# Kernel optimization log

Measured on AMD Instinct MI355X. Metric: run time of the kernel, lower is better.

Reference implementation:

```python
import jax, jax.numpy as jnp
import numpy as np

# config dims (see shape_source)
NO = 8        # Max_Object
NT = 32       # Max_Time
C = 512       # feat_dims
VD = 1024     # visual_dim
RD = 300      # self.nfeat (relation word-vector dim)
H = 4         # headnum
B = 8         # batch
No = NT * 2 * NO      # 512 object-graph nodes
Nr = NT * NO * NO     # 2048 relation-graph nodes


def _glorot(key, shape):
    fan_in = shape[0]
    return jax.random.normal(key, shape, dtype=jnp.float32) / np.sqrt(fan_in)


def setup_inputs() -> dict:
    key = jax.random.key(0)
    ks = jax.random.split(key, 18)
    inp = {
        "Ao": jax.random.uniform(ks[0], (B, No, No), dtype=jnp.float32),
        "srco": jax.random.normal(ks[1], (B, 1, 1, No, VD), dtype=jnp.float32),
        "Ar": jax.random.uniform(ks[2], (B, Nr, Nr), dtype=jnp.float32),
        "srcr": jax.random.normal(ks[3], (B, 1, 1, Nr, RD), dtype=jnp.float32),
        # GraphConvolution weights: gcl_o/gcl2_o and gcl_r/gcl2_r
        "Wo1": _glorot(ks[4], (VD, 1024)),
        "Wo2": _glorot(ks[5], (1024, C)),
        "Wr1": _glorot(ks[6], (RD, 1024)),
        "Wr2": _glorot(ks[7], (1024, C)),
        # MultiHeadAttention (e2n) projections
        "Wq": _glorot(ks[8], (C, C)), "bq": jnp.zeros((C,), jnp.float32),
        "Wk": _glorot(ks[9], (C, C)), "bk": jnp.zeros((C,), jnp.float32),
        "Wv": _glorot(ks[10], (C, C)), "bv": jnp.zeros((C,), jnp.float32),
        "Wp": _glorot(ks[11], (C, C)), "bp": jnp.zeros((C,), jnp.float32),
        # e2n_embed: Linear(2C -> C)
        "We": _glorot(ks[12], (2 * C, C)), "be": jnp.zeros((C,), jnp.float32),
    }
    return inp


def _gcn2(A, x, W1, W2):
    """Two stacked GraphConvolution layers with self-loops: relu((A+I) @ x @ W).
    A: (b,N,N), x: (b,N,Din). Vectorized over batch (torch code loops per-sample)."""
    eye = jnp.eye(A.shape[-1], dtype=A.dtype)
    Ah = A + eye
    h = jax.nn.relu(jnp.einsum('bij,bjd->bid', Ah, x @ W1))
    return jax.nn.relu(jnp.einsum('bij,bjd->bid', Ah, h @ W2))


def _mha(x, Wq, bq, Wk, bk, Wv, bv, Wp, bp):
    """Standard multi-head self-attention. x: (Bseg, S, C)."""
    Bs, S, _ = x.shape
    dh = C // H
    q = (x @ Wq + bq).reshape(Bs, S, H, dh)
    k = (x @ Wk + bk).reshape(Bs, S, H, dh)
    v = (x @ Wv + bv).reshape(Bs, S, H, dh)
    attn = jax.nn.softmax(jnp.einsum('bqhd,bkhd->bhqk', q, k) / np.sqrt(dh), axis=-1)
    o = jnp.einsum('bhqk,bkhd->bqhd', attn, v).reshape(Bs, S, C)
    return o @ Wp + bp


def _forward(Ao, srco, Ar, srcr, Wo1, Wo2, Wr1, Wr2,
             Wq, bq, Wk, bk, Wv, bv, Wp, bp, We, be):
    b = Ao.shape[0]
    # object-graph GCN (torch loops over batch; vectorized here)
    xo = srco[:, 0, 0, :, :VD]                       # (b, No, VD)
    srco_gcn = _gcn2(Ao, xo, Wo1, Wo2)               # (b, No, C)
    out_gcn_o = srco_gcn.reshape(b, NT, 2 * NO, C)
    # relation-graph GCN
    xr = srcr[:, 0, 0]                               # (b, Nr, RD)
    srcr_gcn = _gcn2(Ar, xr, Wr1, Wr2)               # (b, Nr, C)
    out_gcn_r = srcr_gcn.reshape(b, NT, NO * NO, C)
    # compute_e2n: segment-wise MHA over NO-token windows (torch loops over NO)
    r = out_gcn_r.reshape(b * NT, NO, NO, C)
    seg_a = r.reshape(b * NT * NO, NO, C)                      # rows of NOxNO grid
    a = _mha(seg_a, Wq, bq, Wk, bk, Wv, bv, Wp, bp).mean(axis=1)
    a = a.reshape(b * NT, NO, C)
    seg_o = jnp.swapaxes(r, 1, 2).reshape(b * NT * NO, NO, C)  # cols (permute 0,2,1,3)
    o = _mha(seg_o, Wq, bq, Wk, bk, Wv, bv, Wp, bp).mean(axis=1)
    o = o.reshape(b * NT, NO, C)
    tmp = jnp.concatenate([a, o], axis=1)                      # (b*NT, 2*NO, C)
    cat = jnp.concatenate([tmp, out_gcn_o.reshape(b * NT, 2 * NO, C)], axis=-1)
    out_e2n = cat @ We + be
    return out_e2n.reshape(b, NT, 2 * NO, C)


def reference(Ao, srco, Ar, srcr, Wo1, Wo2, Wr1, Wr2,
              Wq, bq, Wk, bk, Wv, bv, Wp, bp, We, be):
    return _forward(Ao, srco, Ar, srcr, Wo1, Wo2, Wr1, Wr2,
                    Wq, bq, Wk, bk, Wv, bv, Wp, bp, We, be)
```

## Files before the change

### kernel.cpp

```cpp
#include <hip/hip_runtime.h>
#include <hip/hip_bf16.h>


typedef __attribute__((ext_vector_type(4))) float f32x4;
typedef __attribute__((ext_vector_type(8))) short bf16x8s;

#define TILE 128
#define BKK 32
#define LDSS 40

__device__ inline void split2(float a, float b, unsigned& h, unsigned& l) {
    __hip_bfloat16 ha = __float2bfloat16(a), hb = __float2bfloat16(b);
    float ra = __bfloat162float(ha), rb = __bfloat162float(hb);
    __hip_bfloat16 la = __float2bfloat16(a - ra), lb = __float2bfloat16(b - rb);
    unsigned short uha = *(unsigned short*)&ha, uhb = *(unsigned short*)&hb;
    unsigned short ula = *(unsigned short*)&la, ulb = *(unsigned short*)&lb;
    h = (unsigned)uha | ((unsigned)uhb << 16);
    l = (unsigned)ula | ((unsigned)ulb << 16);
}

__global__ __launch_bounds__(256) void gemm_split2(
    const float* __restrict__ A, long long sA, int lda,
    const float* __restrict__ BT, long long sBT, int ldbt,
    float* __restrict__ D, long long sD, int ldd,
    const float* __restrict__ addN, long long sAddN, int ldaddN,
    const float* __restrict__ addT, long long sAddT, int ldaddT,
    const float* __restrict__ bias,
    int K, int relu)
{
    __shared__ __hip_bfloat16 Ah[TILE * LDSS], Al[TILE * LDSS];
    __shared__ __hip_bfloat16 Bh[TILE * LDSS], Bl[TILE * LDSS];

    const int tid  = threadIdx.x;
    const int lane = tid & 63;
    const int wave = tid >> 6;
    const int wm   = (wave >> 1) * 64;
    const int wn   = (wave & 1) * 64;
    const int row0 = blockIdx.y * TILE;
    const int col0 = blockIdx.x * TILE;
    const int b    = blockIdx.z;

    const float* Ab = A  + (size_t)b * sA;
    const float* Bb = BT + (size_t)b * sBT;

    f32x4 acc[4][4];
#pragma unroll
    for (int i = 0; i < 4; ++i)
#pragma unroll
        for (int j = 0; j < 4; ++j) acc[i][j] = (f32x4){0.f, 0.f, 0.f, 0.f};

    const int quad = lane >> 4;
    const int l16  = lane & 15;

    for (int k0 = 0; k0 < K; k0 += BKK) {
        __syncthreads();
#pragma unroll
        for (int it = 0; it < 2; ++it) {
            int task = tid + it * 256;
            int m = task >> 2, kq = task & 3;
            const float* ap = Ab + (size_t)(row0 + m) * lda + k0 + kq * 8;
            float4 v0 = *(const float4*)ap;
            float4 v1 = *(const float4*)(ap + 4);
            uint4 H, L;
            split2(v0.x, v0.y, H.x, L.x); split2(v0.z, v0.w, H.y, L.y);
            split2(v1.x, v1.y, H.z, L.z); split2(v1.z, v1.w, H.w, L.w);
            *(uint4*)(&Ah[m * LDSS + kq * 8]) = H;
            *(uint4*)(&Al[m * LDSS + kq * 8]) = L;
        }
#pragma unroll
        for (int it = 0; it < 2; ++it) {
            int task = tid + it * 256;
            int n = task >> 2, kq = task & 3;
            const float* bp = Bb + (size_t)(col0 + n) * ldbt + k0 + kq * 8;
            float4 v0 = *(const float4*)bp;
            float4 v1 = *(const float4*)(bp + 4);
            uint4 H, L;
            split2(v0.x, v0.y, H.x, L.x); split2(v0.z, v0.w, H.y, L.y);
            split2(v1.x, v1.y, H.z, L.z); split2(v1.z, v1.w, H.w, L.w);
            *(uint4*)(&Bh[n * LDSS + kq * 8]) = H;
            *(uint4*)(&Bl[n * LDSS + kq * 8]) = L;
        }
        __syncthreads();

        bf16x8s ah[4], al[4], bh[4], bl[4];
#pragma unroll
        for (int mt = 0; mt < 4; ++mt) {
            int r = (wm + mt * 16 + l16) * LDSS + quad * 8;
            ah[mt] = *(const bf16x8s*)(&Ah[r]);
            al[mt] = *(const bf16x8s*)(&Al[r]);
        }
#pragma unroll
        for (int nt = 0; nt < 4; ++nt) {
            int r = (wn + nt * 16 + l16) * LDSS + quad * 8;
            bh[nt] = *(const bf16x8s*)(&Bh[r]);
            bl[nt] = *(const bf16x8s*)(&Bl[r]);
        }
#pragma unroll
        for (int mt = 0; mt < 4; ++mt)
#pragma unroll
            for (int nt = 0; nt < 4; ++nt) {
                acc[mt][nt] = __builtin_amdgcn_mfma_f32_16x16x32_bf16(ah[mt], bh[nt], acc[mt][nt], 0, 0, 0);
                acc[mt][nt] = __builtin_amdgcn_mfma_f32_16x16x32_bf16(ah[mt], bl[nt], acc[mt][nt], 0, 0, 0);
                acc[mt][nt] = __builtin_amdgcn_mfma_f32_16x16x32_bf16(al[mt], bh[nt], acc[mt][nt], 0, 0, 0);
            }
    }

    float* Db = D + (size_t)b * sD;
    const float* AddN = addN ? addN + (size_t)b * sAddN : nullptr;
    const float* AddT = addT ? addT + (size_t)b * sAddT : nullptr;
#pragma unroll
    for (int mt = 0; mt < 4; ++mt)
#pragma unroll
        for (int nt = 0; nt < 4; ++nt)
#pragma unroll
            for (int r = 0; r < 4; ++r) {
                int m = row0 + wm + mt * 16 + quad * 4 + r;
                int n = col0 + wn + nt * 16 + l16;
                float v = acc[mt][nt][r];
                if (AddN) v += AddN[(size_t)m * ldaddN + n];
                if (AddT) v += AddT[(size_t)n * ldaddT + m];
                if (bias) v += bias[n];
                if (relu && v < 0.f) v = 0.f;
                Db[(size_t)m * ldd + n] = v;
            }
}

__global__ __launch_bounds__(256) void padtrans(
    const float* __restrict__ src, float* __restrict__ dst,
    int R, int C, int Rp, int Cp)
{
    __shared__ float T[64][65];
    const int t = threadIdx.x;
    const int tr = t >> 4, tc = t & 15;
    const int c0 = blockIdx.x * 64, r0 = blockIdx.y * 64;
    const size_t bat = blockIdx.z;
    const float* sb = src + bat * (size_t)R * C;
    float* db = dst + bat * (size_t)Cp * Rp;

#pragma unroll
    for (int i = 0; i < 4; ++i) {
        int rr = tr + i * 16;
        int gr = r0 + rr;
        float v0 = 0.f, v1 = 0.f, v2 = 0.f, v3 = 0.f;
        if (gr < R) {
            int c = c0 + tc * 4;
            const float* s = sb + (size_t)gr * C + c;
            if (c + 0 < C) v0 = s[0];
            if (c + 1 < C) v1 = s[1];
            if (c + 2 < C) v2 = s[2];
            if (c + 3 < C) v3 = s[3];
        }
        T[rr][tc * 4 + 0] = v0; T[rr][tc * 4 + 1] = v1;
        T[rr][tc * 4 + 2] = v2; T[rr][tc * 4 + 3] = v3;
    }
    __syncthreads();
#pragma unroll
    for (int i = 0; i < 4; ++i) {
        int cc = tr + i * 16;
        float4 v = { T[tc * 4 + 0][cc], T[tc * 4 + 1][cc],
                     T[tc * 4 + 2][cc], T[tc * 4 + 3][cc] };
        *(float4*)(db + (size_t)(c0 + cc) * Rp + r0 + tc * 4) = v;
    }
}

__global__ __launch_bounds__(256) void gemm_bf16(
    const __hip_bfloat16* __restrict__ A, long long sA, int lda,
    const __hip_bfloat16* __restrict__ B, long long sB, int ldb,
    void* __restrict__ D, long long sD, int ldd,
    const __hip_bfloat16* __restrict__ addsrc, long long sAdd, int ldadd,
    const float* __restrict__ bias,
    int K, int relu, int outF32)
{
    __shared__ __hip_bfloat16 As[TILE * LDSS];
    __shared__ __hip_bfloat16 Bs[TILE * LDSS];

    const int tid  = threadIdx.x;
    const int lane = tid & 63;
    const int wave = tid >> 6;
    const int wm   = (wave >> 1) * 64;
    const int wn   = (wave & 1) * 64;
    const int row0 = blockIdx.y * TILE;
    const int col0 = blockIdx.x * TILE;
    const int b    = blockIdx.z;

    const __hip_bfloat16* Ab = A + (size_t)b * sA;
    const __hip_bfloat16* Bb = B + (size_t)b * sB;

    f32x4 acc[4][4];
#pragma unroll
    for (int i = 0; i < 4; ++i)
#pragma unroll
        for (int j = 0; j < 4; ++j) acc[i][j] = (f32x4){0.f, 0.f, 0.f, 0.f};

    const int quad = lane >> 4;
    const int l16  = lane & 15;

    for (int k0 = 0; k0 < K; k0 += BKK) {
        __syncthreads();
#pragma unroll
        for (int it = 0; it < 2; ++it) {
            int task = tid + it * 256;
            int m = task >> 2, kq = task & 3;
            uint4 val = *(const uint4*)(Ab + (size_t)(row0 + m) * lda + k0 + kq * 8);
            *(uint4*)(&As[m * LDSS + kq * 8]) = val;
        }
#pragma unroll
        for (int it = 0; it < 2; ++it) {
            int task = tid + it * 256;
            int kk = task >> 4, n8 = task & 15;
            uint4 val = *(const uint4*)(Bb + (size_t)(k0 + kk) * ldb + col0 + n8 * 8);
            const __hip_bfloat16* v16 = (const __hip_bfloat16*)&val;
#pragma unroll
            for (int u = 0; u < 8; ++u)
                Bs[(n8 * 8 + u) * LDSS + kk] = v16[u];
        }
        __syncthreads();

        bf16x8s afrag[4], bfrag[4];
#pragma unroll
        for (int mt = 0; mt < 4; ++mt)
            afrag[mt] = *(const bf16x8s*)(&As[(wm + mt * 16 + l16) * LDSS + quad * 8]);
#pragma unroll
        for (int nt = 0; nt < 4; ++nt)
            bfrag[nt] = *(const bf16x8s*)(&Bs[(wn + nt * 16 + l16) * LDSS + quad * 8]);
#pragma unroll
        for (int mt = 0; mt < 4; ++mt)
#pragma unroll
            for (int nt = 0; nt < 4; ++nt)
                acc[mt][nt] = __builtin_amdgcn_mfma_f32_16x16x32_bf16(
                    afrag[mt], bfrag[nt], acc[mt][nt], 0, 0, 0);
    }

    __hip_bfloat16* Db16 = (__hip_bfloat16*)D + (size_t)b * sD;
    float*          DbF  = (float*)D + (size_t)b * sD;
    const __hip_bfloat16* Addb = addsrc ? addsrc + (size_t)b * sAdd : nullptr;
#pragma unroll
    for (int mt = 0; mt < 4; ++mt)
#pragma unroll
        for (int nt = 0; nt < 4; ++nt)
#pragma unroll
            for (int r = 0; r < 4; ++r) {
                int m = row0 + wm + mt * 16 + quad * 4 + r;
                int n = col0 + wn + nt * 16 + l16;
                float v = acc[mt][nt][r];
                if (Addb) v += __bfloat162float(Addb[(size_t)m * ldadd + n]);
                if (bias) v += bias[n];
                if (relu && v < 0.f) v = 0.f;
                if (outF32) DbF[(size_t)m * ldd + n] = v;
                else        Db16[(size_t)m * ldd + n] = __float2bfloat16(v);
            }
}

__global__ void convert_kernel(const float* __restrict__ src,
                               __hip_bfloat16* __restrict__ dst, int n4)
{
    int i = blockIdx.x * blockDim.x + threadIdx.x;
    if (i >= n4) return;
    float4 v = ((const float4*)src)[i];
    __hip_bfloat16 t0 = __float2bfloat16(v.x), t1 = __float2bfloat16(v.y);
    __hip_bfloat16 t2 = __float2bfloat16(v.z), t3 = __float2bfloat16(v.w);
    ushort4 o = { *(unsigned short*)&t0, *(unsigned short*)&t1,
                  *(unsigned short*)&t2, *(unsigned short*)&t3 };
    ((ushort4*)dst)[i] = o;
}

__global__ __launch_bounds__(256) void attn_kernel(
    const float* __restrict__ q,
    const float* __restrict__ k,
    const float* __restrict__ v,
    __hip_bfloat16* __restrict__ abar)
{
    __shared__ float qs[8][512], ks[8][512], vs[8][512];
    __shared__ float sc[4][8][8];
    __shared__ float wb[4][8];

    const int tid  = threadIdx.x;
    const int mode = blockIdx.y;
    const int g    = blockIdx.x >> 3;
    const int idx  = blockIdx.x & 7;
    const int rowBase = g * 64;

    for (int t = tid; t < 512; t += 256) {
        int p = t >> 6, c8 = (t & 63) * 8;
        int row = (mode == 0) ? (rowBase + idx * 8 + p) : (rowBase + p * 8 + idx);
        const float* qp = q + (size_t)row * 512 + c8;
        const float* kp = k + (size_t)row * 512 + c8;
        const float* vp = v + (size_t)row * 512 + c8;
        *(float4*)(&qs[p][c8])     = *(const float4*)(qp);
        *(float4*)(&qs[p][c8 + 4]) = *(const float4*)(qp + 4);
        *(float4*)(&ks[p][c8])     = *(const float4*)(kp);
        *(float4*)(&ks[p][c8 + 4]) = *(const float4*)(kp + 4);
        *(float4*)(&vs[p][c8])     = *(const float4*)(vp);
        *(float4*)(&vs[p][c8 + 4]) = *(const float4*)(vp + 4);
    }
    __syncthreads();

    {
        int h = tid >> 6, l = tid & 63;
        int i = l >> 3, j = l & 7;
        const float* qrow = &qs[i][h * 128];
        const float* krow = &ks[j][h * 128];
        float s = 0.f;
#pragma unroll
        for (int d = 0; d < 128; d += 4) {
            float4 qa = *(const float4*)(qrow + d);
            float4 kb = *(const float4*)(krow + d);
            s += qa.x * kb.x + qa.y * kb.y + qa.z * kb.z + qa.w * kb.w;
        }
        sc[h][i][j] = s * 0.08838834764831845f;
    }
    __syncthreads();

    if (tid < 32) {
        int h = tid >> 3, i = tid & 7;
        float mx = -1e30f;
#pragma unroll
        for (int j = 0; j < 8; ++j) mx = fmaxf(mx, sc[h][i][j]);
        float e[8], sum = 0.f;
#pragma unroll
        for (int j = 0; j < 8; ++j) { e[j] = __expf(sc[h][i][j] - mx); sum += e[j]; }
        float inv = 1.f / sum;
#pragma unroll
        for (int j = 0; j < 8; ++j) sc[h][i][j] = e[j] * inv;
    }
    __syncthreads();

    if (tid < 32) {
        int h = tid >> 3, j = tid & 7;
        float s = 0.f;
#pragma unroll
        for (int i = 0; i < 8; ++i) s += sc[h][i][j];
        wb[h][j] = s * 0.125f;
    }
    __syncthreads();

    {
        int orow = g * 16 + mode * 8 + idx;
        for (int c = tid; c < 512; c += 256) {
            int h = c >> 7;
            float o = 0.f;
#pragma unroll
            for (int j = 0; j < 8; ++j) o += wb[h][j] * vs[j][c];
            abar[(size_t)orow * 512 + c] = __float2bfloat16(o);
        }
    }
}


extern "C" void kernel_launch(void* const* d_in, const int* in_sizes, int n_in,
                              void* d_out, int out_size, void* d_ws, size_t ws_size,
                              hipStream_t stream)
{
    const float* Ao   = (const float*)d_in[0];
    const float* srco = (const float*)d_in[1];
    const float* Ar   = (const float*)d_in[2];
    const float* srcr = (const float*)d_in[3];
    const float* Wo1  = (const float*)d_in[4];
    const float* Wo2  = (const float*)d_in[5];
    const float* Wr1  = (const float*)d_in[6];
    const float* Wr2  = (const float*)d_in[7];
    const float* Wq   = (const float*)d_in[8];
    const float* bq   = (const float*)d_in[9];
    const float* Wk   = (const float*)d_in[10];
    const float* bk   = (const float*)d_in[11];
    const float* Wv   = (const float*)d_in[12];
    const float* bv   = (const float*)d_in[13];
    const float* Wp   = (const float*)d_in[14];
    const float* bp   = (const float*)d_in[15];
    const float* We   = (const float*)d_in[16];
    const float* be   = (const float*)d_in[17];
    float* out = (float*)d_out;

    char* ws = (char*)d_ws;
    const size_t R0 = 0;
    const size_t R1 = 67108864;
    const size_t R2 = 100663296;
    const size_t R3 = 134217728;
    const size_t R4 = 167772160;
    const size_t R5 = 192937984;

    float* HRf  = (float*)(ws + R0);
    float* qF   = (float*)(ws + R0);
    float* kF   = (float*)(ws + R0 + 33554432);
    float* T2Rf = (float*)(ws + R1);
    float* vF   = (float*)(ws + R1);
    float* Uf   = (float*)(ws + R2);
    float* T2RT = (float*)(ws + R2);
    float* GRf  = (float*)(ws + R3);
    float* XPT  = (float*)(ws + R4);
    __hip_bfloat16* ABAR = (__hip_bfloat16*)(ws + R4);
    float* WPT  = (float*)(ws + R5);
    float* Wr2T = (float*)(ws + R5 + 1310720);
    float* WqT  = (float*)(ws + R5 + 3407872);
    float* WkT  = (float*)(ws + R5 + 4456448);
    float* WvT  = (float*)(ws + R5 + 5505024);

    __hip_bfloat16* TO    = (__hip_bfloat16*)(ws + R2 + 0);
    __hip_bfloat16* HO    = (__hip_bfloat16*)(ws + R2 + 8388608);
    __hip_bfloat16* T2O   = (__hip_bfloat16*)(ws + R2 + 16777216);
    __hip_bfloat16* CAT   = (__hip_bfloat16*)(ws + R2 + 20971520);
    __hip_bfloat16* srcoB = (__hip_bfloat16*)(ws + R2 + 29360128);
    __hip_bfloat16* AoB   = (__hip_bfloat16*)(ws + R2 + 37748736);
    __hip_bfloat16* Wo1B  = (__hip_bfloat16*)(ws + R2 + 41943040);
    __hip_bfloat16* Wo2B  = (__hip_bfloat16*)(ws + R2 + 44040192);
    __hip_bfloat16* WeB   = (__hip_bfloat16*)(ws + R2 + 45088768);
    __hip_bfloat16* WpB   = (__hip_bfloat16*)(ws + R2 + 46137344);

    dim3 blk(256);
    auto cvt = [&](const float* s, __hip_bfloat16* d, int n) {
        convert_kernel<<<dim3((n / 4 + 255) / 256), blk, 0, stream>>>(s, d, n / 4);
    };

    padtrans<<<dim3(6, 32, 8), blk, 0, stream>>>(srcr, XPT, 2048, 300, 2048, 384);
    padtrans<<<dim3(16, 5, 1), blk, 0, stream>>>(Wr1, WPT, 300, 1024, 320, 1024);
    padtrans<<<dim3(8, 16, 1), blk, 0, stream>>>(Wr2, Wr2T, 1024, 512, 1024, 512);
    padtrans<<<dim3(8, 8, 1), blk, 0, stream>>>(Wq, WqT, 512, 512, 512, 512);
    padtrans<<<dim3(8, 8, 1), blk, 0, stream>>>(Wk, WkT, 512, 512, 512, 512);
    padtrans<<<dim3(8, 8, 1), blk, 0, stream>>>(Wv, WvT, 512, 512, 512, 512);

    gemm_split2<<<dim3(3, 16, 8), blk, 0, stream>>>(
        Ar, 2048LL * 2048, 2048, XPT, 384LL * 2048, 2048,
        Uf, 2048LL * 384, 384, nullptr, 0, 0, XPT, 384LL * 2048, 2048,
        nullptr, 2048, 0);
    gemm_split2<<<dim3(8, 128, 1), blk, 0, stream>>>(
        Uf, 0, 384, WPT, 0, 320,
        HRf, 0, 1024, nullptr, 0, 0, nullptr, 0, 0,
        nullptr, 320, 1);
    gemm_split2<<<dim3(4, 128, 1), blk, 0, stream>>>(
        HRf, 0, 1024, Wr2T, 0, 1024,
        T2Rf, 0, 512, nullptr, 0, 0, nullptr, 0, 0,
        nullptr, 1024, 0);
    padtrans<<<dim3(8, 32, 8), blk, 0, stream>>>(T2Rf, T2RT, 2048, 512, 2048, 512);
    gemm_split2<<<dim3(4, 16, 8), blk, 0, stream>>>(
        Ar, 2048LL * 2048, 2048, T2RT, 512LL * 2048, 2048,
        GRf, 2048LL * 512, 512, T2Rf, 2048LL * 512, 512, nullptr, 0, 0,
        nullptr, 2048, 1);
    gemm_split2<<<dim3(4, 128, 1), blk, 0, stream>>>(
        GRf, 0, 512, WqT, 0, 512, qF, 0, 512,
        nullptr, 0, 0, nullptr, 0, 0, bq, 512, 0);
    gemm_split2<<<dim3(4, 128, 1), blk, 0, stream>>>(
        GRf, 0, 512, WkT, 0, 512, kF, 0, 512,
        nullptr, 0, 0, nullptr, 0, 0, bk, 512, 0);
    gemm_split2<<<dim3(4, 128, 1), blk, 0, stream>>>(
        GRf, 0, 512, WvT, 0, 512, vF, 0, 512,
        nullptr, 0, 0, nullptr, 0, 0, bv, 512, 0);
    attn_kernel<<<dim3(2048, 2), blk, 0, stream>>>(qF, kF, vF, ABAR);

    cvt(srco, srcoB, 4194304);
    cvt(Ao, AoB, 2097152);
    cvt(Wo1, Wo1B, 1048576);
    cvt(Wo2, Wo2B, 524288);
    cvt(We, WeB, 524288);
    cvt(Wp, WpB, 262144);
    gemm_bf16<<<dim3(8, 32, 1), blk, 0, stream>>>(srcoB, 0, 1024, Wo1B, 0, 1024,
        TO, 0, 1024, nullptr, 0, 0, nullptr, 1024, 0, 0);
    gemm_bf16<<<dim3(8, 4, 8), blk, 0, stream>>>(AoB, 512LL * 512, 512, TO, 512LL * 1024, 1024,
        HO, 512LL * 1024, 1024, TO, 512LL * 1024, 1024, nullptr, 512, 1, 0);
    gemm_bf16<<<dim3(4, 32, 1), blk, 0, stream>>>(HO, 0, 1024, Wo2B, 0, 512,
        T2O, 0, 512, nullptr, 0, 0, nullptr, 1024, 0, 0);
    gemm_bf16<<<dim3(4, 4, 8), blk, 0, stream>>>(AoB, 512LL * 512, 512, T2O, 512LL * 512, 512,
        (void*)(CAT + 512), 512LL * 1024, 1024, T2O, 512LL * 512, 512, nullptr, 512, 1, 0);
    gemm_bf16<<<dim3(4, 32, 1), blk, 0, stream>>>(ABAR, 0, 512, WpB, 0, 512,
        CAT, 0, 1024, nullptr, 0, 0, bp, 512, 0, 0);
    gemm_bf16<<<dim3(4, 32, 1), blk, 0, stream>>>(CAT, 0, 1024, WeB, 0, 512,
        out, 0, 512, nullptr, 0, 0, be, 1024, 0, 1);
}
```

Measured before the change: 1.203 ms.

## Pre-split fp32 operands into bf16 hi/lo planes and drop V precision

Replaces the fp32-loading split GEMM with a kernel that reads precomputed bf16 high/low planes, so the costly float-to-bf16 splitting happens once per element instead of once per tile reload. Intermediate GEMM outputs are written directly as hi/lo planes, and the T2R transpose now moves 16-bit data. The V projection switches to a plain single-bf16 GEMM on the high plane only, which reduces work but lowers precision for V. Splitting Ar up front adds an extra pass over the large 2048x2048 batched matrix and enlarges the workspace.

Measured after the change: 1.258 ms. +4.6%, slower.

```diff
diff --git a/kernel.cpp b/kernel.cpp
--- a/kernel.cpp
+++ b/kernel.cpp
@@ -9,27 +9,31 @@
 #define BKK 32
 #define LDSS 40
 
-__device__ inline void split2(float a, float b, unsigned& h, unsigned& l) {
-    __hip_bfloat16 ha = __float2bfloat16(a), hb = __float2bfloat16(b);
-    float ra = __bfloat162float(ha), rb = __bfloat162float(hb);
-    __hip_bfloat16 la = __float2bfloat16(a - ra), lb = __float2bfloat16(b - rb);
-    unsigned short uha = *(unsigned short*)&ha, uhb = *(unsigned short*)&hb;
-    unsigned short ula = *(unsigned short*)&la, ulb = *(unsigned short*)&lb;
-    h = (unsigned)uha | ((unsigned)uhb << 16);
-    l = (unsigned)ula | ((unsigned)ulb << 16);
-}
-
-__global__ __launch_bounds__(256) void gemm_split2(
-    const float* __restrict__ A, long long sA, int lda,
-    const float* __restrict__ BT, long long sBT, int ldbt,
-    float* __restrict__ D, long long sD, int ldd,
-    const float* __restrict__ addN, long long sAddN, int ldaddN,
-    const float* __restrict__ addT, long long sAddT, int ldaddT,
+__device__ inline void splt(float v, unsigned short& h, unsigned short& l) {
+    __hip_bfloat16 hb = __float2bfloat16(v);
+    float hf = __bfloat162float(hb);
+    __hip_bfloat16 lb = __float2bfloat16(v - hf);
+    h = *(unsigned short*)&hb;
+    l = *(unsigned short*)&lb;
+}
+
+__global__ __launch_bounds__(256) void gemm3p(
+    const __hip_bfloat16* __restrict__ AH, const __hip_bfloat16* __restrict__ AL,
+    long long sA, int lda,
+    const __hip_bfloat16* __restrict__ BTH, const __hip_bfloat16* __restrict__ BTL,
+    long long sBT, int ldbt,
+    float* __restrict__ DF,
+    __hip_bfloat16* __restrict__ DH, __hip_bfloat16* __restrict__ DL,
+    long long sD, int ldd,
+    const __hip_bfloat16* __restrict__ addNH, const __hip_bfloat16* __restrict__ addNL,
+    long long sAddN, int ldaddN,
+    const __hip_bfloat16* __restrict__ addTH, const __hip_bfloat16* __restrict__ addTL,
+    long long sAddT, int ldaddT,
     const float* __restrict__ bias,
     int K, int relu)
 {
-    __shared__ __hip_bfloat16 Ah[TILE * LDSS], Al[TILE * LDSS];
-    __shared__ __hip_bfloat16 Bh[TILE * LDSS], Bl[TILE * LDSS];
+    __shared__ __hip_bfloat16 Ahs[TILE * LDSS], Als[TILE * LDSS];
+    __shared__ __hip_bfloat16 Bhs[TILE * LDSS], Bls[TILE * LDSS];
 
     const int tid  = threadIdx.x;
     const int lane = tid & 63;
@@ -40,8 +44,10 @@
     const int col0 = blockIdx.x * TILE;
     const int b    = blockIdx.z;
 
-    const float* Ab = A  + (size_t)b * sA;
-    const float* Bb = BT + (size_t)b * sBT;
+    const __hip_bfloat16* AHb = AH + (size_t)b * sA;
+    const __hip_bfloat16* ALb = AL + (size_t)b * sA;
+    const __hip_bfloat16* BHb = BTH + (size_t)b * sBT;
+    const __hip_bfloat16* BLb = BTL + (size_t)b * sBT;
 
     f32x4 acc[4][4];
 #pragma unroll
@@ -58,27 +64,17 @@
         for (int it = 0; it < 2; ++it) {
             int task = tid + it * 256;
             int m = task >> 2, kq = task & 3;
-            const float* ap = Ab + (size_t)(row0 + m) * lda + k0 + kq * 8;
-            float4 v0 = *(const float4*)ap;
-            float4 v1 = *(const float4*)(ap + 4);
-            uint4 H, L;
-            split2(v0.x, v0.y, H.x, L.x); split2(v0.z, v0.w, H.y, L.y);
-            split2(v1.x, v1.y, H.z, L.z); split2(v1.z, v1.w, H.w, L.w);
-            *(uint4*)(&Ah[m * LDSS + kq * 8]) = H;
-            *(uint4*)(&Al[m * LDSS + kq * 8]) = L;
+            size_t go = (size_t)(row0 + m) * lda + k0 + kq * 8;
+            *(uint4*)(&Ahs[m * LDSS + kq * 8]) = *(const uint4*)(AHb + go);
+            *(uint4*)(&Als[m * LDSS + kq * 8]) = *(const uint4*)(ALb + go);
         }
 #pragma unroll
         for (int it = 0; it < 2; ++it) {
             int task = tid + it * 256;
             int n = task >> 2, kq = task & 3;
-            const float* bp = Bb + (size_t)(col0 + n) * ldbt + k0 + kq * 8;
-            float4 v0 = *(const float4*)bp;
-            float4 v1 = *(const float4*)(bp + 4);
-            uint4 H, L;
-            split2(v0.x, v0.y, H.x, L.x); split2(v0.z, v0.w, H.y, L.y);
-            split2(v1.x, v1.y, H.z, L.z); split2(v1.z, v1.w, H.w, L.w);
-            *(uint4*)(&Bh[n * LDSS + kq * 8]) = H;
-            *(uint4*)(&Bl[n * LDSS + kq * 8]) = L;
+            size_t go = (size_t)(col0 + n) * ldbt + k0 + kq * 8;
+            *(uint4*)(&Bhs[n * LDSS + kq * 8]) = *(const uint4*)(BHb + go);
+            *(uint4*)(&Bls[n * LDSS + kq * 8]) = *(const uint4*)(BLb + go);
         }
         __syncthreads();
 
@@ -86,14 +82,14 @@
 #pragma unroll
         for (int mt = 0; mt < 4; ++mt) {
             int r = (wm + mt * 16 + l16) * LDSS + quad * 8;
-            ah[mt] = *(const bf16x8s*)(&Ah[r]);
-            al[mt] = *(const bf16x8s*)(&Al[r]);
+            ah[mt] = *(const bf16x8s*)(&Ahs[r]);
+            al[mt] = *(const bf16x8s*)(&Als[r]);
         }
 #pragma unroll
         for (int nt = 0; nt < 4; ++nt) {
             int r = (wn + nt * 16 + l16) * LDSS + quad * 8;
-            bh[nt] = *(const bf16x8s*)(&Bh[r]);
-            bl[nt] = *(const bf16x8s*)(&Bl[r]);
+            bh[nt] = *(const bf16x8s*)(&Bhs[r]);
+            bl[nt] = *(const bf16x8s*)(&Bls[r]);
         }
 #pragma unroll
         for (int mt = 0; mt < 4; ++mt)
@@ -105,9 +101,13 @@
             }
     }
 
-    float* Db = D + (size_t)b * sD;
-    const float* AddN = addN ? addN + (size_t)b * sAddN : nullptr;
-    const float* AddT = addT ? addT + (size_t)b * sAddT : nullptr;
+    float* DFb = DF ? DF + (size_t)b * sD : nullptr;
+    __hip_bfloat16* DHb = DH ? DH + (size_t)b * sD : nullptr;
+    __hip_bfloat16* DLb = DL ? DL + (size_t)b * sD : nullptr;
+    const __hip_bfloat16* aNH = addNH ? addNH + (size_t)b * sAddN : nullptr;
+    const __hip_bfloat16* aNL = addNL ? addNL + (size_t)b * sAddN : nullptr;
+    const __hip_bfloat16* aTH = addTH ? addTH + (size_t)b * sAddT : nullptr;
+    const __hip_bfloat16* aTL = addTL ? addTL + (size_t)b * sAddT : nullptr;
 #pragma unroll
     for (int mt = 0; mt < 4; ++mt)
 #pragma unroll
@@ -117,17 +117,41 @@
                 int m = row0 + wm + mt * 16 + quad * 4 + r;
                 int n = col0 + wn + nt * 16 + l16;
                 float v = acc[mt][nt][r];
-                if (AddN) v += AddN[(size_t)m * ldaddN + n];
-                if (AddT) v += AddT[(size_t)n * ldaddT + m];
+                if (aNH) v += __bfloat162float(aNH[(size_t)m * ldaddN + n])
+                            + __bfloat162float(aNL[(size_t)m * ldaddN + n]);
+                if (aTH) v += __bfloat162float(aTH[(size_t)n * ldaddT + m])
+                            + __bfloat162float(aTL[(size_t)n * ldaddT + m]);
                 if (bias) v += bias[n];
                 if (relu && v < 0.f) v = 0.f;
-                Db[(size_t)m * ldd + n] = v;
+                if (DFb) DFb[(size_t)m * ldd + n] = v;
+                else {
+                    unsigned short h, l;
+                    splt(v, h, l);
+                    ((unsigned short*)DHb)[(size_t)m * ldd + n] = h;
+                    ((unsigned short*)DLb)[(size_t)m * ldd + n] = l;
+                }
             }
 }
 
-__global__ __launch_bounds__(256) void padtrans(
-    const float* __restrict__ src, float* __restrict__ dst,
-    int R, int C, int Rp, int Cp)
+__global__ void split_planes(const float* __restrict__ src,
+                             __hip_bfloat16* __restrict__ H,
+                             __hip_bfloat16* __restrict__ L, int n8)
+{
+    int i = blockIdx.x * blockDim.x + threadIdx.x;
+    if (i >= n8) return;
+    float4 v0 = ((const float4*)src)[i * 2];
+    float4 v1 = ((const float4*)src)[i * 2 + 1];
+    float vals[8] = {v0.x, v0.y, v0.z, v0.w, v1.x, v1.y, v1.z, v1.w};
+    unsigned short hh[8], ll[8];
+#pragma unroll
+    for (int u = 0; u < 8; ++u) splt(vals[u], hh[u], ll[u]);
+    *(uint4*)((unsigned short*)H + (size_t)i * 8) = *(uint4*)hh;
+    *(uint4*)((unsigned short*)L + (size_t)i * 8) = *(uint4*)ll;
+}
+
+__global__ __launch_bounds__(256) void padtrans_split(
+    const float* __restrict__ src, __hip_bfloat16* __restrict__ dH,
+    __hip_bfloat16* __restrict__ dL, int R, int C, int Rp, int Cp)
 {
     __shared__ float T[64][65];
     const int t = threadIdx.x;
@@ -135,7 +159,8 @@
     const int c0 = blockIdx.x * 64, r0 = blockIdx.y * 64;
     const size_t bat = blockIdx.z;
     const float* sb = src + bat * (size_t)R * C;
-    float* db = dst + bat * (size_t)Cp * Rp;
+    unsigned short* dHb = (unsigned short*)dH + bat * (size_t)Cp * Rp;
+    unsigned short* dLb = (unsigned short*)dL + bat * (size_t)Cp * Rp;
 
 #pragma unroll
     for (int i = 0; i < 4; ++i) {
@@ -157,9 +182,42 @@
 #pragma unroll
     for (int i = 0; i < 4; ++i) {
         int cc = tr + i * 16;
-        float4 v = { T[tc * 4 + 0][cc], T[tc * 4 + 1][cc],
-                     T[tc * 4 + 2][cc], T[tc * 4 + 3][cc] };
-        *(float4*)(db + (size_t)(c0 + cc) * Rp + r0 + tc * 4) = v;
+        unsigned short h[4], l[4];
+#pragma unroll
+        for (int u = 0; u < 4; ++u) splt(T[tc * 4 + u][cc], h[u], l[u]);
+        size_t off = (size_t)(c0 + cc) * Rp + r0 + tc * 4;
+        *(ushort4*)(dHb + off) = *(ushort4*)h;
+        *(ushort4*)(dLb + off) = *(ushort4*)l;
+    }
+}
+
+__global__ __launch_bounds__(256) void trans_bf16(
+    const __hip_bfloat16* __restrict__ sH, const __hip_bfloat16* __restrict__ sL,
+    __hip_bfloat16* __restrict__ dH, __hip_bfloat16* __restrict__ dL,
+    int R, int C)
+{
+    __shared__ unsigned short T[64][68];
+    const int plane = blockIdx.z & 1;
+    const size_t bat = blockIdx.z >> 1;
+    const unsigned short* s = (const unsigned short*)(plane ? sL : sH) + bat * (size_t)R * C;
+    unsigned short* d = (unsigned short*)(plane ? dL : dH) + bat * (size_t)R * C;
+    const int t = threadIdx.x;
+    const int tr = t >> 4, tc = t & 15;
+    const int c0 = blockIdx.x * 64, r0 = blockIdx.y * 64;
+#pragma unroll
+    for (int i = 0; i < 4; ++i) {
+        int rr = tr + i * 16;
+        ushort4 v = *(const ushort4*)(s + (size_t)(r0 + rr) * C + c0 + tc * 4);
+        T[rr][tc * 4 + 0] = v.x; T[rr][tc * 4 + 1] = v.y;
+        T[rr][tc * 4 + 2] = v.z; T[rr][tc * 4 + 3] = v.w;
+    }
+    __syncthreads();
+#pragma unroll
+    for (int i = 0; i < 4; ++i) {
+        int cc = tr + i * 16;
+        ushort4 o = { T[tc * 4 + 0][cc], T[tc * 4 + 1][cc],
+                      T[tc * 4 + 2][cc], T[tc * 4 + 3][cc] };
+        *(ushort4*)(d + (size_t)(c0 + cc) * R + r0 + tc * 4) = o;
     }
 }
 
@@ -372,78 +430,91 @@
     float* out = (float*)d_out;
 
     char* ws = (char*)d_ws;
-    const size_t R0 = 0;
-    const size_t R1 = 67108864;
-    const size_t R2 = 100663296;
-    const size_t R3 = 134217728;
-    const size_t R4 = 167772160;
-    const size_t R5 = 192937984;
-
-    float* HRf  = (float*)(ws + R0);
-    float* qF   = (float*)(ws + R0);
-    float* kF   = (float*)(ws + R0 + 33554432);
-    float* T2Rf = (float*)(ws + R1);
-    float* vF   = (float*)(ws + R1);
-    float* Uf   = (float*)(ws + R2);
-    float* T2RT = (float*)(ws + R2);
-    float* GRf  = (float*)(ws + R3);
-    float* XPT  = (float*)(ws + R4);
-    __hip_bfloat16* ABAR = (__hip_bfloat16*)(ws + R4);
-    float* WPT  = (float*)(ws + R5);
-    float* Wr2T = (float*)(ws + R5 + 1310720);
-    float* WqT  = (float*)(ws + R5 + 3407872);
-    float* WkT  = (float*)(ws + R5 + 4456448);
-    float* WvT  = (float*)(ws + R5 + 5505024);
-
-    __hip_bfloat16* TO    = (__hip_bfloat16*)(ws + R2 + 0);
-    __hip_bfloat16* HO    = (__hip_bfloat16*)(ws + R2 + 8388608);
-    __hip_bfloat16* T2O   = (__hip_bfloat16*)(ws + R2 + 16777216);
-    __hip_bfloat16* CAT   = (__hip_bfloat16*)(ws + R2 + 20971520);
-    __hip_bfloat16* srcoB = (__hip_bfloat16*)(ws + R2 + 29360128);
-    __hip_bfloat16* AoB   = (__hip_bfloat16*)(ws + R2 + 37748736);
-    __hip_bfloat16* Wo1B  = (__hip_bfloat16*)(ws + R2 + 41943040);
-    __hip_bfloat16* Wo2B  = (__hip_bfloat16*)(ws + R2 + 44040192);
-    __hip_bfloat16* WeB   = (__hip_bfloat16*)(ws + R2 + 45088768);
-    __hip_bfloat16* WpB   = (__hip_bfloat16*)(ws + R2 + 46137344);
+    __hip_bfloat16* ArH   = (__hip_bfloat16*)(ws + 0);
+    __hip_bfloat16* ArL   = (__hip_bfloat16*)(ws + 67108864);
+    __hip_bfloat16* XPTH  = (__hip_bfloat16*)(ws + 134217728);
+    __hip_bfloat16* XPTL  = (__hip_bfloat16*)(ws + 146800640);
+    __hip_bfloat16* UH    = (__hip_bfloat16*)(ws + 159383552);
+    __hip_bfloat16* UL    = (__hip_bfloat16*)(ws + 171966464);
+    __hip_bfloat16* HRH   = (__hip_bfloat16*)(ws + 184549376);
+    __hip_bfloat16* HRL   = (__hip_bfloat16*)(ws + 218103808);
+    __hip_bfloat16* T2RH  = (__hip_bfloat16*)(ws + 134217728);
+    __hip_bfloat16* T2RL  = (__hip_bfloat16*)(ws + 150994944);
+    __hip_bfloat16* T2RTH = (__hip_bfloat16*)(ws + 167772160);
+    __hip_bfloat16* T2RTL = (__hip_bfloat16*)(ws + 184549376);
+    __hip_bfloat16* GRH   = (__hip_bfloat16*)(ws + 201326592);
+    __hip_bfloat16* GRL   = (__hip_bfloat16*)(ws + 218103808);
+    float* qF = (float*)(ws + 0);
+    float* kF = (float*)(ws + 33554432);
+    float* vF = (float*)(ws + 67108864);
+    __hip_bfloat16* ABAR  = (__hip_bfloat16*)(ws + 100663296);
+    __hip_bfloat16* TO    = (__hip_bfloat16*)(ws + 104857600);
+    __hip_bfloat16* HO    = (__hip_bfloat16*)(ws + 113246208);
+    __hip_bfloat16* T2O   = (__hip_bfloat16*)(ws + 121634816);
+    __hip_bfloat16* CAT   = (__hip_bfloat16*)(ws + 125829120);
+    __hip_bfloat16* srcoB = (__hip_bfloat16*)(ws + 134217728);
+    __hip_bfloat16* AoB   = (__hip_bfloat16*)(ws + 142606336);
+    __hip_bfloat16* Wo1B  = (__hip_bfloat16*)(ws + 146800640);
+    __hip_bfloat16* Wo2B  = (__hip_bfloat16*)(ws + 148897792);
+    __hip_bfloat16* WeB   = (__hip_bfloat16*)(ws + 149946368);
+    __hip_bfloat16* WpB   = (__hip_bfloat16*)(ws + 150994944);
+    __hip_bfloat16* WPTH  = (__hip_bfloat16*)(ws + 251658240);
+    __hip_bfloat16* WPTL  = (__hip_bfloat16*)(ws + 252313600);
+    __hip_bfloat16* Wr2TH = (__hip_bfloat16*)(ws + 252968960);
+    __hip_bfloat16* Wr2TL = (__hip_bfloat16*)(ws + 254017536);
+    __hip_bfloat16* WqTH  = (__hip_bfloat16*)(ws + 255066112);
+    __hip_bfloat16* WqTL  = (__hip_bfloat16*)(ws + 255590400);
+    __hip_bfloat16* WkTH  = (__hip_bfloat16*)(ws + 256114688);
+    __hip_bfloat16* WkTL  = (__hip_bfloat16*)(ws + 256638976);
+    __hip_bfloat16* WvB   = (__hip_bfloat16*)(ws + 257163264);
 
     dim3 blk(256);
     auto cvt = [&](const float* s, __hip_bfloat16* d, int n) {
         convert_kernel<<<dim3((n / 4 + 255) / 256), blk, 0, stream>>>(s, d, n / 4);
     };
 
-    padtrans<<<dim3(6, 32, 8), blk, 0, stream>>>(srcr, XPT, 2048, 300, 2048, 384);
-    padtrans<<<dim3(16, 5, 1), blk, 0, stream>>>(Wr1, WPT, 300, 1024, 320, 1024);
-    padtrans<<<dim3(8, 16, 1), blk, 0, stream>>>(Wr2, Wr2T, 1024, 512, 1024, 512);
-    padtrans<<<dim3(8, 8, 1), blk, 0, stream>>>(Wq, WqT, 512, 512, 512, 512);
-    padtrans<<<dim3(8, 8, 1), blk, 0, stream>>>(Wk, WkT, 512, 512, 512, 512);
-    padtrans<<<dim3(8, 8, 1), blk, 0, stream>>>(Wv, WvT, 512, 512, 512, 512);
-
-    gemm_split2<<<dim3(3, 16, 8), blk, 0, stream>>>(
-        Ar, 2048LL * 2048, 2048, XPT, 384LL * 2048, 2048,
-        Uf, 2048LL * 384, 384, nullptr, 0, 0, XPT, 384LL * 2048, 2048,
+    split_planes<<<dim3(33554432 / 8 / 256), blk, 0, stream>>>(Ar, ArH, ArL, 33554432 / 8);
+    padtrans_split<<<dim3(6, 32, 8), blk, 0, stream>>>(srcr, XPTH, XPTL, 2048, 300, 2048, 384);
+    padtrans_split<<<dim3(16, 5, 1), blk, 0, stream>>>(Wr1, WPTH, WPTL, 300, 1024, 320, 1024);
+    padtrans_split<<<dim3(8, 16, 1), blk, 0, stream>>>(Wr2, Wr2TH, Wr2TL, 1024, 512, 1024, 512);
+    padtrans_split<<<dim3(8, 8, 1), blk, 0, stream>>>(Wq, WqTH, WqTL, 512, 512, 512, 512);
+    padtrans_split<<<dim3(8, 8, 1), blk, 0, stream>>>(Wk, WkTH, WkTL, 512, 512, 512, 512);
+    cvt(Wv, WvB, 262144);
+
+    gemm3p<<<dim3(3, 16, 8), blk, 0, stream>>>(
+        ArH, ArL, 2048LL * 2048, 2048, XPTH, XPTL, 384LL * 2048, 2048,
+        nullptr, UH, UL, 2048LL * 384, 384,
+        nullptr, nullptr, 0, 0, XPTH, XPTL, 384LL * 2048, 2048,
         nullptr, 2048, 0);
-    gemm_split2<<<dim3(8, 128, 1), blk, 0, stream>>>(
-        Uf, 0, 384, WPT, 0, 320,
-        HRf, 0, 1024, nullptr, 0, 0, nullptr, 0, 0,
+    gemm3p<<<dim3(8, 128, 1), blk, 0, stream>>>(
+        UH, UL, 0, 384, WPTH, WPTL, 0, 320,
+        nullptr, HRH, HRL, 0, 1024,
+        nullptr, nullptr, 0, 0, nullptr, nullptr, 0, 0,
         nullptr, 320, 1);
-    gemm_split2<<<dim3(4, 128, 1), blk, 0, stream>>>(
-        HRf, 0, 1024, Wr2T, 0, 1024,
-        T2Rf, 0, 512, nullptr, 0, 0, nullptr, 0, 0,
+    gemm3p<<<dim3(4, 128, 1), blk, 0, stream>>>(
+        HRH, HRL, 0, 1024, Wr2TH, Wr2TL, 0, 1024,
+        nullptr, T2RH, T2RL, 0, 512,
+        nullptr, nullptr, 0, 0, nullptr, nullptr, 0, 0,
         nullptr, 1024, 0);
-    padtrans<<<dim3(8, 32, 8), blk, 0, stream>>>(T2Rf, T2RT, 2048, 512, 2048, 512);
-    gemm_split2<<<dim3(4, 16, 8), blk, 0, stream>>>(
-        Ar, 2048LL * 2048, 2048, T2RT, 512LL * 2048, 2048,
-        GRf, 2048LL * 512, 512, T2Rf, 2048LL * 512, 512, nullptr, 0, 0,
+    trans_bf16<<<dim3(8, 32, 16), blk, 0, stream>>>(T2RH, T2RL, T2RTH, T2RTL, 2048, 512);
+    gemm3p<<<dim3(4, 16, 8), blk, 0, stream>>>(
+        ArH, ArL, 2048LL * 2048, 2048, T2RTH, T2RTL, 512LL * 2048, 2048,
+        nullptr, GRH, GRL, 2048LL * 512, 512,
+        T2RH, T2RL, 2048LL * 512, 512, nullptr, nullptr, 0, 0,
         nullptr, 2048, 1);
-    gemm_split2<<<dim3(4, 128, 1), blk, 0, stream>>>(
-        GRf, 0, 512, WqT, 0, 512, qF, 0, 512,
-        nullptr, 0, 0, nullptr, 0, 0, bq, 512, 0);
-    gemm_split2<<<dim3(4, 128, 1), blk, 0, stream>>>(
-        GRf, 0, 512, WkT, 0, 512, kF, 0, 512,
-        nullptr, 0, 0, nullptr, 0, 0, bk, 512, 0);
-    gemm_split2<<<dim3(4, 128, 1), blk, 0, stream>>>(
-        GRf, 0, 512, WvT, 0, 512, vF, 0, 512,
-        nullptr, 0, 0, nullptr, 0, 0, bv, 512, 0);
+    gemm3p<<<dim3(4, 128, 1), blk, 0, stream>>>(
+        GRH, GRL, 0, 512, WqTH, WqTL, 0, 512,
+        qF, nullptr, nullptr, 0, 512,
+        nullptr, nullptr, 0, 0, nullptr, nullptr, 0, 0,
+        bq, 512, 0);
+    gemm3p<<<dim3(4, 128, 1), blk, 0, stream>>>(
+        GRH, GRL, 0, 512, WkTH, WkTL, 0, 512,
+        kF, nullptr, nullptr, 0, 512,
+        nullptr, nullptr, 0, 0, nullptr, nullptr, 0, 0,
+        bk, 512, 0);
+    gemm_bf16<<<dim3(4, 128, 1), blk, 0, stream>>>(
+        GRH, 0, 512, WvB, 0, 512, vF, 0, 512,
+        nullptr, 0, 0, bv, 512, 0, 1);
     attn_kernel<<<dim3(2048, 2), blk, 0, stream>>>(qF, kF, vF, ABAR);
 
     cvt(srco, srcoB, 4194304);
```
